# Kernel optimization log

Measured on AMD Instinct MI355X. Metric: run time of the kernel, lower is better.

The kernel has to match this reference:

```python
import jax, jax.numpy as jnp
import numpy as np

NUM_HEADS = 16
WINDOW = 256


def setup_inputs() -> dict:
    key = jax.random.key(0)
    ks = jax.random.split(key, 4)
    B, S, D = 1, 4096, 1024
    scale = 1.0 / np.sqrt(D)  # keep logits sane with random weights
    x = jax.random.normal(ks[0], (B, S, D), dtype=jnp.float32)
    Wq = jax.random.normal(ks[1], (D, D), dtype=jnp.float32) * scale
    Wk = jax.random.normal(ks[2], (D, D), dtype=jnp.float32) * scale
    Wv = jax.random.normal(ks[3], (D, D), dtype=jnp.float32) * scale
    bq = jnp.zeros((D,), dtype=jnp.float32)
    bk = jnp.zeros((D,), dtype=jnp.float32)
    bv = jnp.zeros((D,), dtype=jnp.float32)
    return {"x": x, "Wq": Wq, "bq": bq, "Wk": Wk, "bk": bk, "Wv": Wv, "bv": bv}


def reference(x, Wq, bq, Wk, bk, Wv, bv):
    B, S, D = x.shape
    H = NUM_HEADS
    depth = D // H

    def split_heads(t):
        return t.reshape(B, S, H, depth).transpose(0, 2, 1, 3)  # [B,H,S,depth]

    # torch nn.Linear: y = x @ W.T + b
    Q = split_heads(x @ Wq.T + bq)
    K = split_heads(x @ Wk.T + bk)
    V = split_heads(x @ Wv.T + bv)

    scores = jnp.einsum("bhqd,bhkd->bhqk", Q, K) / jnp.sqrt(jnp.float32(depth))
    idx = jnp.arange(S)
    band = jnp.abs(idx[None, :] - idx[:, None]) <= WINDOW  # [S,S] local window
    scores = jnp.where(band[None, None], scores, -jnp.inf)
    attn = jax.nn.softmax(scores, axis=-1)
    out = jnp.einsum("bhqk,bhkd->bhqd", attn, V)
    return out.transpose(0, 2, 1, 3).reshape(B, S, D)
```

## Files before the change

### kernel.cpp

```cpp
#include <hip/hip_runtime.h>
#include <hip/hip_bf16.h>

typedef __attribute__((ext_vector_type(4))) float f32x4;
typedef __attribute__((ext_vector_type(8))) short s16x8;
typedef __attribute__((ext_vector_type(4))) float float4_t;
typedef __attribute__((ext_vector_type(2))) unsigned int u32x2;

union U8 { s16x8 v; unsigned u[4]; };

__device__ __forceinline__ ushort f2bf(float f) {
  union { float f; unsigned u; } v; v.f = f;
  unsigned r = v.u + 0x7fffu + ((v.u >> 16) & 1u);
  return (ushort)(r >> 16);
}

__device__ __forceinline__ void async_copy16(ushort* lds, const ushort* g) {
  __builtin_amdgcn_global_load_lds(
      (const __attribute__((address_space(1))) unsigned int*)g,
      (__attribute__((address_space(3))) unsigned int*)lds, 16, 0, 0);
}

__device__ __forceinline__ unsigned lds_addr(const void* p) {
  return (unsigned)(unsigned long long)(__attribute__((address_space(3))) const void*)p;
}

#define TRRD(dst, addr, off_lit) \
  asm volatile("ds_read_b64_tr_b16 %0, %1 offset:" #off_lit : "=v"(dst) : "v"(addr))

__global__ __launch_bounds__(256) void convert_kernel(
    const float* __restrict__ x, const float* __restrict__ Wq,
    const float* __restrict__ Wk, const float* __restrict__ Wv,
    ushort* __restrict__ xs, ushort* __restrict__ ws) {
  int b = blockIdx.x;
  if (b < 2048) {
    int c = b * 256 + threadIdx.x;
    int kc = c & 127;
    int m = c >> 7;
    const float4_t* s = (const float4_t*)&x[(size_t)m * 1024 + kc * 8];
    float4_t a0 = s[0], a1 = s[1];
    s16x8 v;
    v[0] = (short)f2bf(a0[0]); v[1] = (short)f2bf(a0[1]);
    v[2] = (short)f2bf(a0[2]); v[3] = (short)f2bf(a0[3]);
    v[4] = (short)f2bf(a1[0]); v[5] = (short)f2bf(a1[1]);
    v[6] = (short)f2bf(a1[2]); v[7] = (short)f2bf(a1[3]);
    int tm = m >> 7, tk = kc >> 3, r = m & 127, c8 = kc & 7;
    *(s16x8*)&xs[((size_t)(tm * 16 + tk) * 128 + r) * 64 + ((c8 ^ (r & 7)) * 8)] = v;
  } else {
    int c = (b - 2048) * 256 + threadIdx.x;
    int kc = c & 127;
    int n = c >> 7;
    int p = n >> 10, nW = n & 1023;
    const float* __restrict__ W = (p == 0) ? Wq : (p == 1) ? Wk : Wv;
    const float4_t* s = (const float4_t*)&W[(size_t)nW * 1024 + kc * 8];
    float4_t a0 = s[0], a1 = s[1];
    s16x8 v;
    v[0] = (short)f2bf(a0[0]); v[1] = (short)f2bf(a0[1]);
    v[2] = (short)f2bf(a0[2]); v[3] = (short)f2bf(a0[3]);
    v[4] = (short)f2bf(a1[0]); v[5] = (short)f2bf(a1[1]);
    v[6] = (short)f2bf(a1[2]); v[7] = (short)f2bf(a1[3]);
    unsigned tn3 = (unsigned)n / 192u;
    unsigned r = (unsigned)n - tn3 * 192u;
    int tk = kc >> 3, c8 = kc & 7;
    *(s16x8*)&ws[((size_t)(tn3 * 16 + tk) * 192 + r) * 64 + ((c8 ^ (r & 7)) * 8)] = v;
  }
}

__global__ __launch_bounds__(512, 2) void qkv_gemm_kernel(
    const ushort* __restrict__ xs, const ushort* __restrict__ wsb,
    const float* __restrict__ bq, const float* __restrict__ bk,
    const float* __restrict__ bv, ushort* __restrict__ qkv) {
  __shared__ ushort lA[2][16384];
  __shared__ ushort lB[2][12288];
  const int t = threadIdx.x;
  const int lane = t & 63, w = t >> 6;
  const int wm = w >> 1, wn = w & 1;
  const int l15 = lane & 15, l4 = lane >> 4;
  const int phys = blockIdx.x;
  const int swz = (phys & 7) * 32 + (phys >> 3);
  const int xcd = swz >> 5, jj = swz & 31;
  const int bm = (xcd >> 1) * 4 + (jj >> 3);
  const int bn = (xcd & 1) * 8 + (jj & 7);

  const ushort* Apan = xs + (size_t)(2 * bm) * 16 * 8192;
  const ushort* Bpan = wsb + (size_t)bn * 16 * 12288;

  f32x4 acc[4][6];
#pragma unroll
  for (int i = 0; i < 4; i++)
#pragma unroll
    for (int j = 0; j < 6; j++) acc[i][j] = (f32x4)0.f;

#define STAGE_A(buf, kt)                                                        \
  do {                                                                          \
    const ushort* s0 = Apan + (size_t)(kt) * 8192;                              \
    const ushort* s1 = Apan + (size_t)(16 + (kt)) * 8192;                       \
    async_copy16(&lA[buf][t * 8], s0 + t * 8);                                  \
    async_copy16(&lA[buf][(t + 512) * 8], s0 + (t + 512) * 8);                  \
    async_copy16(&lA[buf][8192 + t * 8], s1 + t * 8);                           \
    async_copy16(&lA[buf][8192 + (t + 512) * 8], s1 + (t + 512) * 8);           \
  } while (0)
#define STAGE_B(buf, kt)                                                        \
  do {                                                                          \
    const ushort* s2 = Bpan + (size_t)(kt) * 12288;                             \
    async_copy16(&lB[buf][t * 8], s2 + t * 8);                                  \
    async_copy16(&lB[buf][(t + 512) * 8], s2 + (t + 512) * 8);                  \
    async_copy16(&lB[buf][(t + 1024) * 8], s2 + (t + 1024) * 8);                \
  } while (0)

  STAGE_A(0, 0);
  STAGE_B(0, 0);
  asm volatile("s_waitcnt vmcnt(0)");
  __builtin_amdgcn_s_barrier();

  for (int kt = 0; kt < 16; ++kt) {
    const int cur = kt & 1;
    s16x8 af[4], bfr[6];
#pragma unroll
    for (int mi = 0; mi < 4; mi++) {
      int ra = wm * 64 + mi * 16 + l15;
      int g = l4 ^ (ra & 7);
      af[mi] = *(const s16x8*)&lA[cur][ra * 64 + g * 8];
    }
#pragma unroll
    for (int ni = 0; ni < 6; ni++) {
      int rb = wn * 96 + ni * 16 + l15;
      int g = l4 ^ (rb & 7);
      bfr[ni] = *(const s16x8*)&lB[cur][rb * 64 + g * 8];
    }
    if (kt + 1 < 16) {
      STAGE_A(cur ^ 1, kt + 1);
      STAGE_B(cur ^ 1, kt + 1);
    }
    __builtin_amdgcn_s_barrier();
    asm volatile("s_waitcnt lgkmcnt(0)");
    __builtin_amdgcn_sched_barrier(0);
    __builtin_amdgcn_s_setprio(1);
#pragma unroll
    for (int mi = 0; mi < 4; mi++)
#pragma unroll
      for (int ni = 0; ni < 6; ni++)
        acc[mi][ni] = __builtin_amdgcn_mfma_f32_16x16x32_bf16(af[mi], bfr[ni], acc[mi][ni], 0, 0, 0);
    __builtin_amdgcn_s_setprio(0);
    __builtin_amdgcn_s_barrier();
#pragma unroll
    for (int mi = 0; mi < 4; mi++) {
      int ra = wm * 64 + mi * 16 + l15;
      int g = (4 + l4) ^ (ra & 7);
      af[mi] = *(const s16x8*)&lA[cur][ra * 64 + g * 8];
    }
#pragma unroll
    for (int ni = 0; ni < 6; ni++) {
      int rb = wn * 96 + ni * 16 + l15;
      int g = (4 + l4) ^ (rb & 7);
      bfr[ni] = *(const s16x8*)&lB[cur][rb * 64 + g * 8];
    }
    __builtin_amdgcn_s_barrier();
    asm volatile("s_waitcnt lgkmcnt(0)");
    __builtin_amdgcn_sched_barrier(0);
    __builtin_amdgcn_s_setprio(1);
#pragma unroll
    for (int mi = 0; mi < 4; mi++)
#pragma unroll
      for (int ni = 0; ni < 6; ni++)
        acc[mi][ni] = __builtin_amdgcn_mfma_f32_16x16x32_bf16(af[mi], bfr[ni], acc[mi][ni], 0, 0, 0);
    __builtin_amdgcn_s_setprio(0);
    asm volatile("s_waitcnt vmcnt(0)");
    __builtin_amdgcn_s_barrier();
  }
#undef STAGE_A
#undef STAGE_B

#pragma unroll
  for (int ni = 0; ni < 6; ni++) {
    int col = bn * 192 + wn * 96 + ni * 16 + l15;
    int p = col >> 10;
    const float* bias = (p == 0) ? bq : (p == 1) ? bk : bv;
    float b = bias[col & 1023];
    float qscale = (p == 0) ? 0.125f * 1.44269504f : 1.0f;
    int h = (col >> 6) & 15, dd = col & 63;
    size_t base = ((size_t)(p * 16 + h) * 4096) * 64 + dd;
#pragma unroll
    for (int mi = 0; mi < 4; mi++) {
#pragma unroll
      for (int r = 0; r < 4; r++) {
        int s = bm * 256 + wm * 64 + mi * 16 + l4 * 4 + r;
        float v = (acc[mi][ni][r] + b) * qscale;
        qkv[base + (size_t)s * 64] = f2bf(v);
      }
    }
  }
}

__global__ __launch_bounds__(512) void attn_local_kernel(
    const ushort* __restrict__ qkv, float* __restrict__ out) {
  __shared__ ushort lds[2][2][4096];
  const int bid = blockIdx.x;
  const int wid = (bid & 7) * 64 + (bid >> 3);
  const int h = wid >> 5;
  const int q0 = (wid & 31) << 7;
  const int t = threadIdx.x;
  const int lane = t & 63, w = t >> 6;
  const int l15 = lane & 15, l4 = lane >> 4;
  const int qw = q0 + w * 16;
  const int myq = qw + l15;

  const ushort* __restrict__ Q = qkv;
  const ushort* __restrict__ K = qkv + (size_t)16 * 4096 * 64;
  const ushort* __restrict__ V = K + (size_t)16 * 4096 * 64;

  s16x8 qf[2];
  {
    const ushort* qp = &Q[((size_t)h * 4096 + myq) * 64];
    qf[0] = *(const s16x8*)&qp[l4 * 8];
    qf[1] = *(const s16x8*)&qp[32 + l4 * 8];
  }

  U8 ones;
  {
    unsigned w1 = (l15 == 0) ? 0x3F803F80u : 0u;
    ones.u[0] = w1; ones.u[1] = w1; ones.u[2] = w1; ones.u[3] = w1;
  }

  f32x4 oacc[5];
#pragma unroll
  for (int i = 0; i < 5; i++) oacc[i] = (f32x4)0.f;
  float mrow = -1e30f;

  const unsigned vtr0 = lds_addr(&lds[0][1][0]) +
      (unsigned)(l4 * 1024 + (l15 >> 2) * 128 + (l15 & 3) * 8);

  int kstart = q0 - 256; if (kstart < 0) kstart = 0;
  int kend = q0 + 384; if (kend > 4096) kend = 4096;

#define STAGE_KV(buf, kb)                                                      \
  do {                                                                         \
    const ushort* Kg = &K[((size_t)h * 4096 + (kb)) * 64];                     \
    const ushort* Vg = &V[((size_t)h * 4096 + (kb)) * 64];                     \
    int off = t * 8;                                                           \
    int row = off >> 6;                                                        \
    int c8 = (off >> 3) & 7;                                                   \
    async_copy16(&lds[buf][0][off], &Kg[row * 64 + ((c8 ^ (row & 7)) * 8)]);   \
    async_copy16(&lds[buf][1][off], &Vg[off]);                                 \
  } while (0)

  STAGE_KV(0, kstart);
  asm volatile("s_waitcnt vmcnt(0)");
  __builtin_amdgcn_s_barrier();

  for (int kb = kstart; kb < kend; kb += 64) {
    const int cur = ((kb - kstart) >> 6) & 1;
    if (kb + 64 < kend) {
      if (cur) STAGE_KV(0, kb + 64); else STAGE_KV(1, kb + 64);
    }
    bool active = (kb + 63 >= qw - 256) && (kb <= qw + 15 + 256);
    if (active) {
      const ushort* lK = &lds[cur][0][0];
      f32x4 st[4];
#pragma unroll
      for (int tt = 0; tt < 4; tt++) st[tt] = (f32x4)0.f;
      __builtin_amdgcn_s_setprio(1);
#pragma unroll
      for (int tt = 0; tt < 4; tt++) {
#pragma unroll
        for (int kc = 0; kc < 2; kc++) {
          int rowk = tt * 16 + l15;
          int g = (kc * 4 + l4) ^ (rowk & 7);
          s16x8 kf = *(const s16x8*)&lK[rowk * 64 + g * 8];
          st[tt] = __builtin_amdgcn_mfma_f32_16x16x32_bf16(kf, qf[kc], st[tt], 0, 0, 0);
        }
      }
      __builtin_amdgcn_s_setprio(0);
      float pe[4][4];
      const bool interior = (kb >= qw - 241) && (kb <= qw + 193);
      if (interior) {
#pragma unroll
        for (int tt = 0; tt < 4; tt++)
#pragma unroll
          for (int r = 0; r < 4; r++) pe[tt][r] = st[tt][r];
      } else {
#pragma unroll
        for (int tt = 0; tt < 4; tt++)
#pragma unroll
          for (int r = 0; r < 4; r++) {
            int key = kb + tt * 16 + l4 * 4 + r;
            pe[tt][r] = ((unsigned)(myq - key + 256) <= 512u) ? st[tt][r] : -3e38f;
          }
      }
      float m0 = fmaxf(fmaxf(pe[0][0], pe[0][1]), fmaxf(pe[0][2], pe[0][3]));
      float m1 = fmaxf(fmaxf(pe[1][0], pe[1][1]), fmaxf(pe[1][2], pe[1][3]));
      float m2 = fmaxf(fmaxf(pe[2][0], pe[2][1]), fmaxf(pe[2][2], pe[2][3]));
      float m3 = fmaxf(fmaxf(pe[3][0], pe[3][1]), fmaxf(pe[3][2], pe[3][3]));
      float rm = fmaxf(fmaxf(m0, m1), fmaxf(m2, m3));
      rm = fmaxf(rm, __shfl_xor(rm, 16));
      rm = fmaxf(rm, __shfl_xor(rm, 32));
      if (__any(rm > mrow + 8.0f)) {
        float mn = fmaxf(mrow, rm);
        float sc = __builtin_amdgcn_exp2f(mrow - mn);
        mrow = mn;
        float scr[4];
#pragma unroll
        for (int r = 0; r < 4; r++) scr[r] = __shfl(sc, l4 * 4 + r);
#pragma unroll
        for (int db = 0; db < 5; db++)
#pragma unroll
          for (int r = 0; r < 4; r++) oacc[db][r] *= scr[r];
      }
      unsigned pk[4][2];
#pragma unroll
      for (int tt = 0; tt < 4; tt++) {
        float e0 = __builtin_amdgcn_exp2f(pe[tt][0] - mrow);
        float e1 = __builtin_amdgcn_exp2f(pe[tt][1] - mrow);
        float e2 = __builtin_amdgcn_exp2f(pe[tt][2] - mrow);
        float e3 = __builtin_amdgcn_exp2f(pe[tt][3] - mrow);
        asm("v_cvt_pk_bf16_f32 %0, %1, %2" : "=v"(pk[tt][0]) : "v"(e0), "v"(e1));
        asm("v_cvt_pk_bf16_f32 %0, %1, %2" : "=v"(pk[tt][1]) : "v"(e2), "v"(e3));
      }

      const unsigned vtr = vtr0 + (unsigned)cur * 16384u;
#pragma unroll
      for (int c = 0; c < 2; c++) {
        u32x2 t00, t01, t10, t11, t20, t21, t30, t31;
        if (c == 0) {
          TRRD(t00, vtr, 0);    TRRD(t01, vtr, 512);
          TRRD(t10, vtr, 32);   TRRD(t11, vtr, 544);
          TRRD(t20, vtr, 64);   TRRD(t21, vtr, 576);
          TRRD(t30, vtr, 96);   TRRD(t31, vtr, 608);
        } else {
          TRRD(t00, vtr, 4096); TRRD(t01, vtr, 4608);
          TRRD(t10, vtr, 4128); TRRD(t11, vtr, 4640);
          TRRD(t20, vtr, 4160); TRRD(t21, vtr, 4672);
          TRRD(t30, vtr, 4192); TRRD(t31, vtr, 4704);
        }
        const int srcA = ((lane & 16) << 1) | l15;
        const int srcB = srcA + 16;
        const int tsel = (lane >> 5) & 1;
        unsigned x0 = (unsigned)__shfl((int)pk[2 * c][0], srcA);
        unsigned y0 = (unsigned)__shfl((int)pk[2 * c + 1][0], srcA);
        unsigned x1 = (unsigned)__shfl((int)pk[2 * c][1], srcA);
        unsigned y1 = (unsigned)__shfl((int)pk[2 * c + 1][1], srcA);
        unsigned x2 = (unsigned)__shfl((int)pk[2 * c][0], srcB);
        unsigned y2 = (unsigned)__shfl((int)pk[2 * c + 1][0], srcB);
        unsigned x3 = (unsigned)__shfl((int)pk[2 * c][1], srcB);
        unsigned y3 = (unsigned)__shfl((int)pk[2 * c + 1][1], srcB);
        U8 pf;
        pf.u[0] = tsel ? y0 : x0;
        pf.u[1] = tsel ? y1 : x1;
        pf.u[2] = tsel ? y2 : x2;
        pf.u[3] = tsel ? y3 : x3;
        asm volatile("s_waitcnt lgkmcnt(0)");
        __builtin_amdgcn_sched_barrier(0);
        U8 vf0, vf1, vf2, vf3;
        vf0.u[0] = t00[0]; vf0.u[1] = t00[1]; vf0.u[2] = t01[0]; vf0.u[3] = t01[1];
        vf1.u[0] = t10[0]; vf1.u[1] = t10[1]; vf1.u[2] = t11[0]; vf1.u[3] = t11[1];
        vf2.u[0] = t20[0]; vf2.u[1] = t20[1]; vf2.u[2] = t21[0]; vf2.u[3] = t21[1];
        vf3.u[0] = t30[0]; vf3.u[1] = t30[1]; vf3.u[2] = t31[0]; vf3.u[3] = t31[1];
        __builtin_amdgcn_s_setprio(1);
        oacc[0] = __builtin_amdgcn_mfma_f32_16x16x32_bf16(pf.v, vf0.v, oacc[0], 0, 0, 0);
        oacc[1] = __builtin_amdgcn_mfma_f32_16x16x32_bf16(pf.v, vf1.v, oacc[1], 0, 0, 0);
        oacc[2] = __builtin_amdgcn_mfma_f32_16x16x32_bf16(pf.v, vf2.v, oacc[2], 0, 0, 0);
        oacc[3] = __builtin_amdgcn_mfma_f32_16x16x32_bf16(pf.v, vf3.v, oacc[3], 0, 0, 0);
        oacc[4] = __builtin_amdgcn_mfma_f32_16x16x32_bf16(pf.v, ones.v, oacc[4], 0, 0, 0);
        __builtin_amdgcn_s_setprio(0);
      }
    }
    asm volatile("s_waitcnt vmcnt(0)");
    __builtin_amdgcn_s_barrier();
  }
#undef STAGE_KV
  float linv[4];
#pragma unroll
  for (int r = 0; r < 4; r++) linv[r] = 1.0f / __shfl(oacc[4][r], lane & 48);
#pragma unroll
  for (int db = 0; db < 4; db++)
#pragma unroll
    for (int r = 0; r < 4; r++) {
      int s = qw + l4 * 4 + r;
      out[(size_t)s * 1024 + h * 64 + db * 16 + l15] = oacc[db][r] * linv[r];
    }
}

extern "C" void kernel_launch(void* const* d_in, const int* in_sizes, int n_in,
                              void* d_out, int out_size, void* d_ws, size_t ws_size,
                              hipStream_t stream) {
  const float* x  = (const float*)d_in[0];
  const float* Wq = (const float*)d_in[1];
  const float* bq = (const float*)d_in[2];
  const float* Wk = (const float*)d_in[3];
  const float* bk = (const float*)d_in[4];
  const float* Wv = (const float*)d_in[5];
  const float* bv = (const float*)d_in[6];

  ushort* qkv = (ushort*)d_ws;
  ushort* xs  = (ushort*)((char*)d_ws + (size_t)25165824);
  ushort* wsb = xs + (size_t)4096 * 1024;
  float* out = (float*)d_out;

  convert_kernel<<<3584, 256, 0, stream>>>(x, Wq, Wk, Wv, xs, wsb);
  qkv_gemm_kernel<<<256, 512, 0, stream>>>(xs, wsb, bq, bk, bv, qkv);
  attn_local_kernel<<<512, 512, 0, stream>>>(qkv, out);
}
```

Before: 69.21 us.

## Switch local attention to 32x32x16 MFMA with 32 queries per wave

Rewrites the local-window attention kernel to use 32x32x16 bf16 MFMA tiles. Each wave now handles 32 queries, so a block has 4 waves and 256 threads instead of 8 waves and 512. The P-fragment shuffles are replaced with v_permlane32_swap, and the K/V staging loop now issues two copies per thread. The goal is fewer MFMA issues and less cross-lane shuffle overhead per score tile, at the cost of fewer waves per block and larger accumulators (more registers).

```diff
diff --git a/kernel.cpp b/kernel.cpp
--- a/kernel.cpp
+++ b/kernel.cpp
@@ -2,6 +2,7 @@
 #include <hip/hip_bf16.h>
 
 typedef __attribute__((ext_vector_type(4))) float f32x4;
+typedef __attribute__((ext_vector_type(16))) float f32x16;
 typedef __attribute__((ext_vector_type(8))) short s16x8;
 typedef __attribute__((ext_vector_type(4))) float float4_t;
 typedef __attribute__((ext_vector_type(2))) unsigned int u32x2;
@@ -191,56 +192,57 @@
   }
 }
 
-__global__ __launch_bounds__(512) void attn_local_kernel(
+__global__ __launch_bounds__(256) void attn_local_kernel(
     const ushort* __restrict__ qkv, float* __restrict__ out) {
   __shared__ ushort lds[2][2][4096];
   const int bid = blockIdx.x;
   const int wid = (bid & 7) * 64 + (bid >> 3);
-  const int h = wid >> 5;
+  const int hd = wid >> 5;
   const int q0 = (wid & 31) << 7;
   const int t = threadIdx.x;
   const int lane = t & 63, w = t >> 6;
-  const int l15 = lane & 15, l4 = lane >> 4;
-  const int qw = q0 + w * 16;
-  const int myq = qw + l15;
+  const int l15 = lane & 15, l31 = lane & 31;
+  const int b4 = (lane >> 4) & 1, hf = lane >> 5;
+  const int qw = q0 + w * 32;
+  const int myq = qw + l31;
 
   const ushort* __restrict__ Q = qkv;
   const ushort* __restrict__ K = qkv + (size_t)16 * 4096 * 64;
   const ushort* __restrict__ V = K + (size_t)16 * 4096 * 64;
 
-  s16x8 qf[2];
+  s16x8 qf[4];
   {
-    const ushort* qp = &Q[((size_t)h * 4096 + myq) * 64];
-    qf[0] = *(const s16x8*)&qp[l4 * 8];
-    qf[1] = *(const s16x8*)&qp[32 + l4 * 8];
+    const ushort* qp = &Q[((size_t)hd * 4096 + myq) * 64];
+#pragma unroll
+    for (int kc = 0; kc < 4; kc++) qf[kc] = *(const s16x8*)&qp[16 * kc + 8 * hf];
   }
 
   U8 ones;
   {
-    unsigned w1 = (l15 == 0) ? 0x3F803F80u : 0u;
+    unsigned w1 = (l31 == 0) ? 0x3F803F80u : 0u;
     ones.u[0] = w1; ones.u[1] = w1; ones.u[2] = w1; ones.u[3] = w1;
   }
 
-  f32x4 oacc[5];
-#pragma unroll
-  for (int i = 0; i < 5; i++) oacc[i] = (f32x4)0.f;
+  f32x16 oa0 = (f32x16)0.f, oa1 = (f32x16)0.f, oden = (f32x16)0.f;
   float mrow = -1e30f;
 
   const unsigned vtr0 = lds_addr(&lds[0][1][0]) +
-      (unsigned)(l4 * 1024 + (l15 >> 2) * 128 + (l15 & 3) * 8);
+      (unsigned)(hf * 1024 + (l15 >> 2) * 128 + b4 * 32 + (l15 & 3) * 8);
 
   int kstart = q0 - 256; if (kstart < 0) kstart = 0;
   int kend = q0 + 384; if (kend > 4096) kend = 4096;
 
 #define STAGE_KV(buf, kb)                                                      \
   do {                                                                         \
-    const ushort* Kg = &K[((size_t)h * 4096 + (kb)) * 64];                     \
-    const ushort* Vg = &V[((size_t)h * 4096 + (kb)) * 64];                     \
-    int off = t * 8;                                                           \
-    int row = off >> 6;                                                        \
-    int c8 = (off >> 3) & 7;                                                   \
-    async_copy16(&lds[buf][0][off], &Kg[row * 64 + ((c8 ^ (row & 7)) * 8)]);   \
-    async_copy16(&lds[buf][1][off], &Vg[off]);                                 \
+    const ushort* Kg = &K[((size_t)hd * 4096 + (kb)) * 64];                    \
+    const ushort* Vg = &V[((size_t)hd * 4096 + (kb)) * 64];                    \
+    _Pragma("unroll") for (int i = 0; i < 2; i++) {                            \
+      int off = i * 2048 + t * 8;                                              \
+      int row = off >> 6;                                                      \
+      int c8s = (off >> 3) & 7;                                                \
+      async_copy16(&lds[buf][0][off], &Kg[row * 64 + ((c8s ^ (row & 7)) * 8)]);\
+      async_copy16(&lds[buf][1][off], &Vg[off]);                               \
+    }                                                                          \
   } while (0)
 
   STAGE_KV(0, kstart);
@@ -252,131 +254,106 @@
     if (kb + 64 < kend) {
       if (cur) STAGE_KV(0, kb + 64); else STAGE_KV(1, kb + 64);
     }
-    bool active = (kb + 63 >= qw - 256) && (kb <= qw + 15 + 256);
+    bool active = (kb + 63 >= qw - 256) && (kb <= qw + 31 + 256);
     if (active) {
       const ushort* lK = &lds[cur][0][0];
-      f32x4 st[4];
-#pragma unroll
-      for (int tt = 0; tt < 4; tt++) st[tt] = (f32x4)0.f;
+      f32x16 st0 = (f32x16)0.f, st1 = (f32x16)0.f;
       __builtin_amdgcn_s_setprio(1);
 #pragma unroll
-      for (int tt = 0; tt < 4; tt++) {
-#pragma unroll
-        for (int kc = 0; kc < 2; kc++) {
-          int rowk = tt * 16 + l15;
-          int g = (kc * 4 + l4) ^ (rowk & 7);
-          s16x8 kf = *(const s16x8*)&lK[rowk * 64 + g * 8];
-          st[tt] = __builtin_amdgcn_mfma_f32_16x16x32_bf16(kf, qf[kc], st[tt], 0, 0, 0);
+      for (int kc = 0; kc < 4; kc++) {
+        int c8 = 2 * kc + hf;
+        int r0 = l31;
+        s16x8 kf0 = *(const s16x8*)&lK[r0 * 64 + ((c8 ^ (r0 & 7)) * 8)];
+        st0 = __builtin_amdgcn_mfma_f32_32x32x16_bf16(kf0, qf[kc], st0, 0, 0, 0);
+        int r1 = 32 + l31;
+        s16x8 kf1 = *(const s16x8*)&lK[r1 * 64 + ((c8 ^ (r1 & 7)) * 8)];
+        st1 = __builtin_amdgcn_mfma_f32_32x32x16_bf16(kf1, qf[kc], st1, 0, 0, 0);
+      }
+      __builtin_amdgcn_s_setprio(0);
+      const bool interior = (kb >= qw - 225) && (kb <= qw + 193);
+      if (!interior) {
+        int base0 = myq - kb - 4 * hf + 256;
+#pragma unroll
+        for (int r = 0; r < 16; r++) {
+          int ko = (r & 3) + 8 * (r >> 2);
+          if (!((unsigned)(base0 - ko) <= 512u)) st0[r] = -3e38f;
+          if (!((unsigned)(base0 - 32 - ko) <= 512u)) st1[r] = -3e38f;
         }
       }
-      __builtin_amdgcn_s_setprio(0);
-      float pe[4][4];
-      const bool interior = (kb >= qw - 241) && (kb <= qw + 193);
-      if (interior) {
-#pragma unroll
-        for (int tt = 0; tt < 4; tt++)
-#pragma unroll
-          for (int r = 0; r < 4; r++) pe[tt][r] = st[tt][r];
-      } else {
-#pragma unroll
-        for (int tt = 0; tt < 4; tt++)
-#pragma unroll
-          for (int r = 0; r < 4; r++) {
-            int key = kb + tt * 16 + l4 * 4 + r;
-            pe[tt][r] = ((unsigned)(myq - key + 256) <= 512u) ? st[tt][r] : -3e38f;
-          }
-      }
-      float m0 = fmaxf(fmaxf(pe[0][0], pe[0][1]), fmaxf(pe[0][2], pe[0][3]));
-      float m1 = fmaxf(fmaxf(pe[1][0], pe[1][1]), fmaxf(pe[1][2], pe[1][3]));
-      float m2 = fmaxf(fmaxf(pe[2][0], pe[2][1]), fmaxf(pe[2][2], pe[2][3]));
-      float m3 = fmaxf(fmaxf(pe[3][0], pe[3][1]), fmaxf(pe[3][2], pe[3][3]));
-      float rm = fmaxf(fmaxf(m0, m1), fmaxf(m2, m3));
-      rm = fmaxf(rm, __shfl_xor(rm, 16));
+      float rm;
+      {
+        float a = fmaxf(fmaxf(st0[0], st0[1]), fmaxf(st0[2], st0[3]));
+        float b = fmaxf(fmaxf(st0[4], st0[5]), fmaxf(st0[6], st0[7]));
+        float c = fmaxf(fmaxf(st0[8], st0[9]), fmaxf(st0[10], st0[11]));
+        float d = fmaxf(fmaxf(st0[12], st0[13]), fmaxf(st0[14], st0[15]));
+        float e = fmaxf(fmaxf(st1[0], st1[1]), fmaxf(st1[2], st1[3]));
+        float f = fmaxf(fmaxf(st1[4], st1[5]), fmaxf(st1[6], st1[7]));
+        float g = fmaxf(fmaxf(st1[8], st1[9]), fmaxf(st1[10], st1[11]));
+        float h2 = fmaxf(fmaxf(st1[12], st1[13]), fmaxf(st1[14], st1[15]));
+        rm = fmaxf(fmaxf(fmaxf(a, b), fmaxf(c, d)), fmaxf(fmaxf(e, f), fmaxf(g, h2)));
+      }
       rm = fmaxf(rm, __shfl_xor(rm, 32));
       if (__any(rm > mrow + 8.0f)) {
         float mn = fmaxf(mrow, rm);
         float sc = __builtin_amdgcn_exp2f(mrow - mn);
         mrow = mn;
-        float scr[4];
-#pragma unroll
-        for (int r = 0; r < 4; r++) scr[r] = __shfl(sc, l4 * 4 + r);
-#pragma unroll
-        for (int db = 0; db < 5; db++)
-#pragma unroll
-          for (int r = 0; r < 4; r++) oacc[db][r] *= scr[r];
-      }
-      unsigned pk[4][2];
-#pragma unroll
-      for (int tt = 0; tt < 4; tt++) {
-        float e0 = __builtin_amdgcn_exp2f(pe[tt][0] - mrow);
-        float e1 = __builtin_amdgcn_exp2f(pe[tt][1] - mrow);
-        float e2 = __builtin_amdgcn_exp2f(pe[tt][2] - mrow);
-        float e3 = __builtin_amdgcn_exp2f(pe[tt][3] - mrow);
-        asm("v_cvt_pk_bf16_f32 %0, %1, %2" : "=v"(pk[tt][0]) : "v"(e0), "v"(e1));
-        asm("v_cvt_pk_bf16_f32 %0, %1, %2" : "=v"(pk[tt][1]) : "v"(e2), "v"(e3));
-      }
-
+        int srcB = (lane & 32); srcB += srcB >> 3;
+#pragma unroll
+        for (int r = 0; r < 16; r++) {
+          float scr = __shfl(sc, srcB + (r & 3) + 8 * (r >> 2));
+          oa0[r] *= scr; oa1[r] *= scr; oden[r] *= scr;
+        }
+      }
       const unsigned vtr = vtr0 + (unsigned)cur * 16384u;
-#pragma unroll
-      for (int c = 0; c < 2; c++) {
-        u32x2 t00, t01, t10, t11, t20, t21, t30, t31;
-        if (c == 0) {
-          TRRD(t00, vtr, 0);    TRRD(t01, vtr, 512);
-          TRRD(t10, vtr, 32);   TRRD(t11, vtr, 544);
-          TRRD(t20, vtr, 64);   TRRD(t21, vtr, 576);
-          TRRD(t30, vtr, 96);   TRRD(t31, vtr, 608);
-        } else {
-          TRRD(t00, vtr, 4096); TRRD(t01, vtr, 4608);
-          TRRD(t10, vtr, 4128); TRRD(t11, vtr, 4640);
-          TRRD(t20, vtr, 4160); TRRD(t21, vtr, 4672);
-          TRRD(t30, vtr, 4192); TRRD(t31, vtr, 4704);
-        }
-        const int srcA = ((lane & 16) << 1) | l15;
-        const int srcB = srcA + 16;
-        const int tsel = (lane >> 5) & 1;
-        unsigned x0 = (unsigned)__shfl((int)pk[2 * c][0], srcA);
-        unsigned y0 = (unsigned)__shfl((int)pk[2 * c + 1][0], srcA);
-        unsigned x1 = (unsigned)__shfl((int)pk[2 * c][1], srcA);
-        unsigned y1 = (unsigned)__shfl((int)pk[2 * c + 1][1], srcA);
-        unsigned x2 = (unsigned)__shfl((int)pk[2 * c][0], srcB);
-        unsigned y2 = (unsigned)__shfl((int)pk[2 * c + 1][0], srcB);
-        unsigned x3 = (unsigned)__shfl((int)pk[2 * c][1], srcB);
-        unsigned y3 = (unsigned)__shfl((int)pk[2 * c + 1][1], srcB);
-        U8 pf;
-        pf.u[0] = tsel ? y0 : x0;
-        pf.u[1] = tsel ? y1 : x1;
-        pf.u[2] = tsel ? y2 : x2;
-        pf.u[3] = tsel ? y3 : x3;
-        asm volatile("s_waitcnt lgkmcnt(0)");
-        __builtin_amdgcn_sched_barrier(0);
-        U8 vf0, vf1, vf2, vf3;
-        vf0.u[0] = t00[0]; vf0.u[1] = t00[1]; vf0.u[2] = t01[0]; vf0.u[3] = t01[1];
-        vf1.u[0] = t10[0]; vf1.u[1] = t10[1]; vf1.u[2] = t11[0]; vf1.u[3] = t11[1];
-        vf2.u[0] = t20[0]; vf2.u[1] = t20[1]; vf2.u[2] = t21[0]; vf2.u[3] = t21[1];
-        vf3.u[0] = t30[0]; vf3.u[1] = t30[1]; vf3.u[2] = t31[0]; vf3.u[3] = t31[1];
-        __builtin_amdgcn_s_setprio(1);
-        oacc[0] = __builtin_amdgcn_mfma_f32_16x16x32_bf16(pf.v, vf0.v, oacc[0], 0, 0, 0);
-        oacc[1] = __builtin_amdgcn_mfma_f32_16x16x32_bf16(pf.v, vf1.v, oacc[1], 0, 0, 0);
-        oacc[2] = __builtin_amdgcn_mfma_f32_16x16x32_bf16(pf.v, vf2.v, oacc[2], 0, 0, 0);
-        oacc[3] = __builtin_amdgcn_mfma_f32_16x16x32_bf16(pf.v, vf3.v, oacc[3], 0, 0, 0);
-        oacc[4] = __builtin_amdgcn_mfma_f32_16x16x32_bf16(pf.v, ones.v, oacc[4], 0, 0, 0);
-        __builtin_amdgcn_s_setprio(0);
-      }
+#define PVC(STV, RB, O0, O1, O2, O3)                                           \
+  do {                                                                         \
+    u32x2 ta, tb, tc2, td;                                                     \
+    TRRD(ta, vtr, O0); TRRD(tb, vtr, O1); TRRD(tc2, vtr, O2); TRRD(td, vtr, O3);\
+    float e0 = __builtin_amdgcn_exp2f(STV[RB + 0] - mrow);                     \
+    float e1 = __builtin_amdgcn_exp2f(STV[RB + 1] - mrow);                     \
+    float e2 = __builtin_amdgcn_exp2f(STV[RB + 2] - mrow);                     \
+    float e3 = __builtin_amdgcn_exp2f(STV[RB + 3] - mrow);                     \
+    float e4 = __builtin_amdgcn_exp2f(STV[RB + 4] - mrow);                     \
+    float e5 = __builtin_amdgcn_exp2f(STV[RB + 5] - mrow);                     \
+    float e6 = __builtin_amdgcn_exp2f(STV[RB + 6] - mrow);                     \
+    float e7 = __builtin_amdgcn_exp2f(STV[RB + 7] - mrow);                     \
+    unsigned a0, a1, b0, b1;                                                   \
+    asm("v_cvt_pk_bf16_f32 %0, %1, %2" : "=v"(a0) : "v"(e0), "v"(e1));         \
+    asm("v_cvt_pk_bf16_f32 %0, %1, %2" : "=v"(a1) : "v"(e2), "v"(e3));         \
+    asm("v_cvt_pk_bf16_f32 %0, %1, %2" : "=v"(b0) : "v"(e4), "v"(e5));         \
+    asm("v_cvt_pk_bf16_f32 %0, %1, %2" : "=v"(b1) : "v"(e6), "v"(e7));         \
+    asm volatile("v_permlane32_swap_b32 %0, %1" : "+v"(a0), "+v"(b0));         \
+    asm volatile("v_permlane32_swap_b32 %0, %1" : "+v"(a1), "+v"(b1));         \
+    U8 pa; pa.u[0] = a0; pa.u[1] = a1; pa.u[2] = b0; pa.u[3] = b1;             \
+    asm volatile("s_waitcnt lgkmcnt(0)");                                      \
+    __builtin_amdgcn_sched_barrier(0);                                         \
+    U8 vf0, vf1;                                                               \
+    vf0.u[0] = ta[0]; vf0.u[1] = ta[1]; vf0.u[2] = tb[0]; vf0.u[3] = tb[1];    \
+    vf1.u[0] = tc2[0]; vf1.u[1] = tc2[1]; vf1.u[2] = td[0]; vf1.u[3] = td[1];  \
+    __builtin_amdgcn_s_setprio(1);                                             \
+    oa0 = __builtin_amdgcn_mfma_f32_32x32x16_bf16(pa.v, vf0.v, oa0, 0, 0, 0);  \
+    oa1 = __builtin_amdgcn_mfma_f32_32x32x16_bf16(pa.v, vf1.v, oa1, 0, 0, 0);  \
+    oden = __builtin_amdgcn_mfma_f32_32x32x16_bf16(pa.v, ones.v, oden, 0, 0, 0);\
+    __builtin_amdgcn_s_setprio(0);                                             \
+  } while (0)
+      PVC(st0, 0, 0, 512, 64, 576);
+      PVC(st0, 8, 2048, 2560, 2112, 2624);
+      PVC(st1, 0, 4096, 4608, 4160, 4672);
+      PVC(st1, 8, 6144, 6656, 6208, 6720);
+#undef PVC
     }
     asm volatile("s_waitcnt vmcnt(0)");
     __builtin_amdgcn_s_barrier();
   }
 #undef STAGE_KV
-  float linv[4];
-#pragma unroll
-  for (int r = 0; r < 4; r++) linv[r] = 1.0f / __shfl(oacc[4][r], lane & 48);
-#pragma unroll
-  for (int db = 0; db < 4; db++)
-#pragma unroll
-    for (int r = 0; r < 4; r++) {
-      int s = qw + l4 * 4 + r;
-      out[(size_t)s * 1024 + h * 64 + db * 16 + l15] = oacc[db][r] * linv[r];
-    }
+#pragma unroll
+  for (int r = 0; r < 16; r++) {
+    float den = __shfl(oden[r], lane & 32);
+    float linv = 1.0f / den;
+    int s = qw + (r & 3) + 8 * (r >> 2) + 4 * hf;
+    out[(size_t)s * 1024 + hd * 64 + l31] = oa0[r] * linv;
+    out[(size_t)s * 1024 + hd * 64 + 32 + l31] = oa1[r] * linv;
+  }
 }
 
 extern "C" void kernel_launch(void* const* d_in, const int* in_sizes, int n_in,
@@ -397,5 +374,5 @@
 
   convert_kernel<<<3584, 256, 0, stream>>>(x, Wq, Wk, Wv, xs, wsb);
   qkv_gemm_kernel<<<256, 512, 0, stream>>>(xs, wsb, bq, bk, bv, qkv);
-  attn_local_kernel<<<512, 512, 0, stream>>>(qkv, out);
-}
+  attn_local_kernel<<<512, 256, 0, stream>>>(qkv, out);
+}
```

Measured after the change: 67.28 us. 1.03x faster.
